# Kernel optimization log

Measured on AMD Instinct MI355X. Metric: run time of the kernel, lower is better.

The kernel has to match this reference:

```python
import jax, jax.numpy as jnp
import numpy as np

B, S = 32, 128
E_NUM, SKILL, D_K, D_E, D_A = 4000, 256, 128, 128, 128
AT_NUM, IT_NUM = 1000, 1000
GAMMA = 0.03


def _lin(key, out_d, in_d):
    # xavier-normal style init
    w = jax.random.normal(key, (out_d, in_d), jnp.float32) * (2.0 / (in_d + out_d)) ** 0.5
    b = jnp.zeros((out_d,), jnp.float32)
    return w, b


def setup_inputs() -> dict:
    key = jax.random.key(0)
    ks = jax.random.split(key, 16)
    exercise_id = jax.random.randint(ks[0], (B, S), 0, E_NUM, jnp.int32)
    ans_time = jax.random.randint(ks[1], (B, S), 0, AT_NUM, jnp.int32)
    interval_time = jax.random.randint(ks[2], (B, S), 0, IT_NUM, jnp.int32)
    answer_value = jax.random.randint(ks[3], (B, S), 0, 2, jnp.int32)
    # enhanced q-matrix: binary with zeros replaced by gamma
    qmask = jax.random.bernoulli(ks[4], 0.1, (E_NUM, SKILL))
    q_matrix = jnp.where(qmask, 1.0, GAMMA).astype(jnp.float32)
    ex_table = jax.random.normal(ks[5], (E_NUM, D_E), jnp.float32)
    at_table = jax.random.normal(ks[6], (AT_NUM, D_K), jnp.float32)
    it_table = jax.random.normal(ks[7], (IT_NUM, D_K), jnp.float32)
    W1, b1 = _lin(ks[8], D_K, D_E + D_K + D_A)   # learning_embed_layer
    Wl, bl = _lin(ks[9], D_K, 4 * D_K)           # learning_layer
    Wg, bg = _lin(ks[10], D_K, 4 * D_K)          # learning_gate
    Wf, bf = _lin(ks[11], D_K, 3 * D_K)          # forgetting_gate
    Wp, bp = _lin(ks[12], D_K, 2 * D_K)          # predicting_layer
    # xavier-uniform initial knowledge state, shared across batch
    lim = (6.0 / (SKILL + D_K)) ** 0.5
    h0 = jax.random.uniform(ks[13], (SKILL, D_K), jnp.float32, -lim, lim)
    return {"exercise_id": exercise_id, "ans_time": ans_time,
            "interval_time": interval_time, "answer_value": answer_value,
            "q_matrix": q_matrix, "ex_table": ex_table, "at_table": at_table,
            "it_table": it_table, "W1": W1, "b1": b1, "Wl": Wl, "bl": bl,
            "Wg": Wg, "bg": bg, "Wf": Wf, "bf": bf, "Wp": Wp, "bp": bp, "h0": h0}


def _forward(exercise_id, ans_time, interval_time, answer_value, q_matrix,
             ex_table, at_table, it_table, W1, b1, Wl, bl, Wg, bg, Wf, bf,
             Wp, bp, h0):
    b, s = exercise_id.shape
    ex = ex_table[exercise_id]                       # (B,S,d_e)
    at = at_table[ans_time]                          # (B,S,d_k)
    it = it_table[interval_time]                     # (B,S,d_k)
    ans = jnp.broadcast_to(answer_value.astype(ex.dtype)[..., None], (b, s, D_A))
    le = jnp.concatenate([ex, at, ans], -1) @ W1.T + b1   # learning embedding (B,S,d_k)
    kv = q_matrix[exercise_id]                       # knowledge vectors (B,S,skill)

    h_pre = jnp.broadcast_to(h0, (b,) + h0.shape)    # (B,skill,d_k)
    h_tilde_pre = jnp.einsum('bs,bsd->bd', kv[:, 0], h_pre)
    learning_pre = jnp.zeros((b, D_K), ex.dtype)

    def step(carry, xs):
        h_pre, h_tilde_pre, learning_pre = carry
        lv, itv, kv_t, kv_next, ex_next = xs
        x4 = jnp.concatenate([learning_pre, itv, lv, h_tilde_pre], -1)
        lg = jnp.tanh(x4 @ Wl.T + bl)
        gate = jax.nn.sigmoid(x4 @ Wg.T + bg)
        LG = gate * (lg + 1.0) * 0.5                 # (B,d_k)
        LG_tilde = kv_t[:, :, None] * LG[:, None, :] # outer product addressing (B,skill,d_k)
        x3 = jnp.concatenate([h_pre,
                              jnp.broadcast_to(LG[:, None, :], h_pre.shape),
                              jnp.broadcast_to(itv[:, None, :], h_pre.shape)], -1)
        f = jax.nn.sigmoid(x3 @ Wf.T + bf)           # forget gate per skill
        h = LG_tilde + f * h_pre                     # updated knowledge state
        h_tilde = jnp.einsum('bs,bsd->bd', kv_next, h)
        pred = jax.nn.sigmoid(jnp.concatenate([ex_next, h_tilde], -1) @ Wp.T + bp)
        return (h, h_tilde, lv), pred

    sw = lambda a: jnp.swapaxes(a, 0, 1)
    xs = (sw(le[:, :-1]), sw(it[:, 1:]), sw(kv[:, :-1]), sw(kv[:, 1:]), sw(ex[:, 1:]))
    _, preds = jax.lax.scan(step, (h_pre, h_tilde_pre, learning_pre), xs)
    return jnp.swapaxes(preds, 0, 1)                 # (B, S-1, d_k)


def reference(exercise_id, ans_time, interval_time, answer_value, q_matrix,
              ex_table, at_table, it_table, W1, b1, Wl, bl, Wg, bg, Wf, bf,
              Wp, bp, h0):
    return _forward(exercise_id, ans_time, interval_time, answer_value, q_matrix,
                    ex_table, at_table, it_table, W1, b1, Wl, bl, Wg, bg, Wf, bf,
                    Wp, bp, h0)
```

## Files before the change

kernel.cpp:

```cpp
#include <hip/hip_runtime.h>

typedef unsigned int u32;
typedef unsigned short u16;
typedef unsigned long long u64;
typedef u16 u16x8 __attribute__((ext_vector_type(8)));
typedef u16 u16x4 __attribute__((ext_vector_type(4)));
typedef __bf16 bf16x8 __attribute__((ext_vector_type(8)));
typedef __bf16 bf16x4v __attribute__((ext_vector_type(4)));
typedef float f32x4 __attribute__((ext_vector_type(4)));
typedef float f32x2 __attribute__((ext_vector_type(2)));

#define B_SZ 32
#define S_SZ 128
#define T_SZ 127
#define DK 128
#define SKILL 256
#define SQTR 64
#define RL 136
#define PP 68
#define NPAIR 8
#define SPIN_CAP (1 << 18)

__device__ __forceinline__ u16x4 cvt4(f32x4 v) {
    return __builtin_bit_cast(u16x4, __builtin_convertvector(v, bf16x4v));
}
__device__ __forceinline__ u16x8 cvt8(f32x4 a, f32x4 b) {
    u16x4 x = cvt4(a), y = cvt4(b);
    u16x8 r;
    r[0]=x[0]; r[1]=x[1]; r[2]=x[2]; r[3]=x[3];
    r[4]=y[0]; r[5]=y[1]; r[6]=y[2]; r[7]=y[3];
    return r;
}
__device__ __forceinline__ u16 bfu(float x) {
    return __builtin_bit_cast(u16, (__bf16)x);
}
__device__ __forceinline__ float sigm(float x) {
    float e = __builtin_amdgcn_exp2f(-1.44269504f * x);
    return __builtin_amdgcn_rcpf(1.f + e);
}
__device__ __forceinline__ float tanh_f(float x) {
    float e = __builtin_amdgcn_exp2f(-2.88539008f * x);
    return 2.f * __builtin_amdgcn_rcpf(1.f + e) - 1.f;
}
__device__ __forceinline__ f32x4 mfma16(u16x8 a, u16x8 bb, f32x4 c) {
    return __builtin_amdgcn_mfma_f32_16x16x32_bf16(
        __builtin_bit_cast(bf16x8, a), __builtin_bit_cast(bf16x8, bb), c, 0, 0, 0);
}
__device__ __forceinline__ float pval(u64 p) {
    return __builtin_bit_cast(float, (u32)p);
}

__global__ __launch_bounds__(256) void k_le(
    const int* __restrict__ eid, const int* __restrict__ atime,
    const int* __restrict__ ansv, const float* __restrict__ ex_t,
    const float* __restrict__ at_t, const float* __restrict__ W1,
    const float* __restrict__ b1, float* __restrict__ le_ws)
{
    const int tid = threadIdx.x;
    const int o = tid & 127;
    const int gi = __builtin_amdgcn_readfirstlane(tid >> 7);
    const int p0 = blockIdx.x * NPAIR + gi * 4;
    int eP[4], aP[4];
    float avP[4];
    #pragma unroll
    for (int i = 0; i < 4; ++i) {
        int p = p0 + i, b = p / T_SZ, t = p - b * T_SZ;
        int idx = b * S_SZ + t;
        eP[i] = eid[idx];
        aP[i] = atime[idx];
        avP[i] = (float)ansv[idx];
    }
    const float* wr = W1 + o * 384;
    const float bias = b1[o];
    float acc[4] = {bias, bias, bias, bias};
    #pragma unroll 4
    for (int k4 = 0; k4 < 32; ++k4) {
        f32x4 w = *(const f32x4*)(wr + 4 * k4);
        #pragma unroll
        for (int i = 0; i < 4; ++i) {
            f32x4 x = *(const f32x4*)(ex_t + eP[i] * DK + 4 * k4);
            acc[i] += w[0] * x[0] + w[1] * x[1] + w[2] * x[2] + w[3] * x[3];
        }
    }
    #pragma unroll 4
    for (int k4 = 32; k4 < 64; ++k4) {
        f32x4 w = *(const f32x4*)(wr + 4 * k4);
        #pragma unroll
        for (int i = 0; i < 4; ++i) {
            f32x4 x = *(const f32x4*)(at_t + aP[i] * DK + 4 * k4 - 128);
            acc[i] += w[0] * x[0] + w[1] * x[1] + w[2] * x[2] + w[3] * x[3];
        }
    }
    float wsum = 0.f;
    #pragma unroll 4
    for (int k4 = 64; k4 < 96; ++k4) {
        f32x4 w = *(const f32x4*)(wr + 4 * k4);
        wsum += w[0] + w[1] + w[2] + w[3];
    }
    #pragma unroll
    for (int i = 0; i < 4; ++i)
        le_ws[(p0 + i) * DK + o] = acc[i] + avP[i] * wsum;
}

__global__ __launch_bounds__(256) void k_pre(
    const int* __restrict__ itime, const float* __restrict__ it_t,
    const float* __restrict__ Wl, const float* __restrict__ blv,
    const float* __restrict__ Wg, const float* __restrict__ bgv,
    const float* __restrict__ Wf, const float* __restrict__ bfv,
    const float* __restrict__ le_ws,
    float* __restrict__ PRE_l, float* __restrict__ PRE_g, float* __restrict__ PRE_f)
{
    const int tid = threadIdx.x;
    const int o = tid & 127;
    const int gi = __builtin_amdgcn_readfirstlane(tid >> 7);
    const int p0 = blockIdx.x * NPAIR + gi * 4;
    int ivP[4], lpOff[4];
    float mP[4];
    #pragma unroll
    for (int i = 0; i < 4; ++i) {
        int p = p0 + i, b = p / T_SZ, t = p - b * T_SZ;
        ivP[i] = itime[b * S_SZ + t + 1];
        mP[i] = (t == 0) ? 0.f : 1.f;
        lpOff[i] = ((t == 0) ? p : p - 1) * DK;
    }
    const float* wl = Wl + o * 512;
    const float* wg = Wg + o * 512;
    const float bl0 = blv[o], bg0 = bgv[o];
    float al[4] = {bl0, bl0, bl0, bl0};
    float ag[4] = {bg0, bg0, bg0, bg0};
    #pragma unroll 4
    for (int k4 = 0; k4 < 32; ++k4) {
        f32x4 w  = *(const f32x4*)(wl + 4 * k4);
        f32x4 w2 = *(const f32x4*)(wg + 4 * k4);
        #pragma unroll
        for (int i = 0; i < 4; ++i) {
            f32x4 x = *(const f32x4*)(le_ws + lpOff[i] + 4 * k4);
            #pragma unroll
            for (int j = 0; j < 4; ++j) {
                float xv = x[j] * mP[i];
                al[i] += w[j] * xv;
                ag[i] += w2[j] * xv;
            }
        }
    }
    #pragma unroll 4
    for (int k4 = 0; k4 < 32; ++k4) {
        f32x4 w  = *(const f32x4*)(wl + 128 + 4 * k4);
        f32x4 w2 = *(const f32x4*)(wg + 128 + 4 * k4);
        #pragma unroll
        for (int i = 0; i < 4; ++i) {
            f32x4 x = *(const f32x4*)(it_t + ivP[i] * DK + 4 * k4);
            #pragma unroll
            for (int j = 0; j < 4; ++j) {
                al[i] += w[j] * x[j];
                ag[i] += w2[j] * x[j];
            }
        }
    }
    #pragma unroll 4
    for (int k4 = 0; k4 < 32; ++k4) {
        f32x4 w  = *(const f32x4*)(wl + 256 + 4 * k4);
        f32x4 w2 = *(const f32x4*)(wg + 256 + 4 * k4);
        #pragma unroll
        for (int i = 0; i < 4; ++i) {
            f32x4 x = *(const f32x4*)(le_ws + (p0 + i) * DK + 4 * k4);
            #pragma unroll
            for (int j = 0; j < 4; ++j) {
                al[i] += w[j] * x[j];
                ag[i] += w2[j] * x[j];
            }
        }
    }
    const float bf0 = bfv[o];
    float af[4] = {bf0, bf0, bf0, bf0};
    const float* wf = Wf + o * 384 + 256;
    #pragma unroll 4
    for (int k4 = 0; k4 < 32; ++k4) {
        f32x4 w = *(const f32x4*)(wf + 4 * k4);
        #pragma unroll
        for (int i = 0; i < 4; ++i) {
            f32x4 x = *(const f32x4*)(it_t + ivP[i] * DK + 4 * k4);
            af[i] += w[0] * x[0] + w[1] * x[1] + w[2] * x[2] + w[3] * x[3];
        }
    }
    #pragma unroll
    for (int i = 0; i < 4; ++i) {
        size_t idx = (size_t)(p0 + i) * DK + o;
        PRE_l[idx] = al[i];
        PRE_g[idx] = ag[i];
        PRE_f[idx] = af[i];
    }
}

__global__ __launch_bounds__(512, 1) void k_main(
    const int* __restrict__ eid, const float* __restrict__ qmat,
    const float* __restrict__ Wl, const float* __restrict__ Wg,
    const float* __restrict__ Wf, const float* __restrict__ h0,
    const float* __restrict__ PRE_l, const float* __restrict__ PRE_g,
    const float* __restrict__ PRE_f, float* __restrict__ ht_ws,
    u64* __restrict__ xbuf)
{
    extern __shared__ char smem[];
    u16*   hS   = (u16*)smem;
    float* part = (float*)(smem + 17408);
    u16*   htbf = (u16*)(smem + 52224);
    u16*   LGb  = (u16*)(smem + 52736);
    float* LGf  = (float*)(smem + 53248);
    float* cS   = (float*)(smem + 53760);

    const int b    = blockIdx.x;
    const int qid  = blockIdx.y;
    const int tid  = threadIdx.x;
    const int w    = tid >> 6;
    const int lane = tid & 63;
    const int quad = lane >> 4;
    const int l4   = lane & 15;
    const int ih   = w & 1;
    const int jh   = w >> 1;

    u64* xq = xbuf + (size_t)b * 1024;
    const int qa = (qid + 1) & 3, qb2 = (qid + 2) & 3, qc = (qid + 3) & 3;

    u16x8 afr[4][4];
    #pragma unroll
    for (int mt = 0; mt < 4; ++mt)
        #pragma unroll
        for (int kt = 0; kt < 4; ++kt) {
            const float* p = Wf + (64 * ih + 16 * mt + l4) * 384 + 32 * kt + quad * 8;
            afr[mt][kt] = cvt8(*(const f32x4*)p, *(const f32x4*)(p + 4));
        }
    u16x8 azf[2][4];
    #pragma unroll
    for (int mt = 0; mt < 2; ++mt)
        #pragma unroll
        for (int kt = 0; kt < 4; ++kt) {
            int d = 16 * w + 8 * mt + (l4 >> 1);
            const float* base = (l4 & 1) ? Wg : Wl;
            const float* p = base + d * 512 + 384 + 32 * kt + quad * 8;
            azf[mt][kt] = cvt8(*(const f32x4*)p, *(const f32x4*)(p + 4));
        }
    u16x8 acf[4];
    #pragma unroll
    for (int kt = 0; kt < 4; ++kt) {
        const float* p = Wf + (16 * w + l4) * 384 + 128 + 32 * kt + quad * 8;
        acf[kt] = cvt8(*(const f32x4*)p, *(const f32x4*)(p + 4));
    }

    const int sl = 16 * jh + l4;
    f32x4 hreg[4];
    #pragma unroll
    for (int mt = 0; mt < 4; ++mt) {
        int d0 = 64 * ih + 16 * mt + quad * 4;
        f32x4 hv = *(const f32x4*)(h0 + (SQTR * qid + sl) * DK + d0);
        hreg[mt] = hv;
        *(u16x4*)(hS + sl * RL + d0) = cvt4(hv);
    }

    float kvt = qmat[eid[b * S_SZ] * SKILL + SQTR * qid + sl];

    f32x4 accF[4];

    {
        float htp[16];
        #pragma unroll
        for (int mt = 0; mt < 4; ++mt)
            #pragma unroll
            for (int r = 0; r < 4; ++r)
                htp[mt * 4 + r] = kvt * hreg[mt][r];
        #pragma unroll
        for (int mt = 0; mt < 4; ++mt)
            #pragma unroll
            for (int r = 0; r < 4; ++r)
                part[(64 * ih + 16 * mt + quad * 4 + r) * PP + jh * 16 + l4] = htp[mt * 4 + r];
        __syncthreads();
        int d = tid >> 2, kq = tid & 3;
        const float* pp = part + d * PP + kq * 16;
        float v = 0.f;
        #pragma unroll
        for (int i4 = 0; i4 < 4; ++i4) {
            f32x4 x = *(const f32x4*)(pp + 4 * i4);
            v += x[0] + x[1] + x[2] + x[3];
        }
        v += __shfl_xor(v, 1, 64);
        v += __shfl_xor(v, 2, 64);
        if (kq == 0) {
            u64 pkt = ((u64)1u << 32) | (u64)__builtin_bit_cast(u32, v);
            __hip_atomic_store(xq + qid * 256 + 128 + d, pkt,
                               __ATOMIC_RELAXED, __HIP_MEMORY_SCOPE_AGENT);
        }
        asm volatile("" ::: "memory");
        #pragma unroll
        for (int mt = 0; mt < 4; ++mt)
            accF[mt] = (f32x4){0.f, 0.f, 0.f, 0.f};
        {
            const u16* bp = hS + sl * RL + quad * 8;
            u16x8 bfr[4];
            #pragma unroll
            for (int kt = 0; kt < 4; ++kt) bfr[kt] = *(const u16x8*)(bp + kt * 32);
            #pragma unroll
            for (int mt = 0; mt < 4; ++mt)
                #pragma unroll
                for (int kt = 0; kt < 4; ++kt)
                    accF[mt] = mfma16(afr[mt][kt], bfr[kt], accF[mt]);
        }
        if (kq == 0) {
            u64 pa, pb, pc;
            int spins = 0;
            do {
                pa = __hip_atomic_load(xq + qa * 256 + 128 + d, __ATOMIC_RELAXED, __HIP_MEMORY_SCOPE_AGENT);
                pb = __hip_atomic_load(xq + qb2 * 256 + 128 + d, __ATOMIC_RELAXED, __HIP_MEMORY_SCOPE_AGENT);
                pc = __hip_atomic_load(xq + qc * 256 + 128 + d, __ATOMIC_RELAXED, __HIP_MEMORY_SCOPE_AGENT);
                if ((u32)(pa >> 32) >= 1u && (u32)(pb >> 32) >= 1u && (u32)(pc >> 32) >= 1u) break;
                if (spins > 64) __builtin_amdgcn_s_sleep(1);
            } while (++spins < SPIN_CAP);
            float va = pval(pa), vb = pval(pb), vc = pval(pc);
            float v0 = (qid == 0) ? v : (qid == 3) ? va : (qid == 2) ? vb : vc;
            float v1 = (qid == 1) ? v : (qid == 0) ? va : (qid == 3) ? vb : vc;
            float v2 = (qid == 2) ? v : (qid == 1) ? va : (qid == 0) ? vb : vc;
            float v3 = (qid == 3) ? v : (qid == 2) ? va : (qid == 1) ? vb : vc;
            float vt = ((v0 + v1) + v2) + v3;
            float hf = (float)(__bf16)vt;
            htbf[d] = bfu(vt);
            htbf[128 + d] = bfu(vt - hf);
        }
        __syncthreads();
    }

    for (int t = 0; t < T_SZ; ++t) {
        const size_t tb = (size_t)(b * T_SZ + t) * DK;
        float kvn = qmat[eid[b * S_SZ + t + 1] * SKILL + SQTR * qid + sl];
        f32x2 pl[2], pg[2];
        #pragma unroll
        for (int mt = 0; mt < 2; ++mt) {
            int d0 = 16 * w + 8 * mt + 2 * quad;
            pl[mt] = *(const f32x2*)(PRE_l + tb + d0);
            pg[mt] = *(const f32x2*)(PRE_g + tb + d0);
        }
        f32x4 pf = *(const f32x4*)(PRE_f + tb + 16 * w + quad * 4);

        f32x4 accZ[2];
        accZ[0] = (f32x4){0.f, 0.f, 0.f, 0.f};
        accZ[1] = (f32x4){0.f, 0.f, 0.f, 0.f};
        #pragma unroll
        for (int kt = 0; kt < 4; ++kt) {
            u16x8 bh = *(const u16x8*)(htbf + 32 * kt + quad * 8);
            u16x8 bl = *(const u16x8*)(htbf + 128 + 32 * kt + quad * 8);
            #pragma unroll
            for (int mt = 0; mt < 2; ++mt) {
                accZ[mt] = mfma16(azf[mt][kt], bh, accZ[mt]);
                accZ[mt] = mfma16(azf[mt][kt], bl, accZ[mt]);
            }
        }
        #pragma unroll
        for (int mt = 0; mt < 2; ++mt) {
            u32 hpack = 0, lpack = 0;
            f32x2 fpack;
            #pragma unroll
            for (int rp = 0; rp < 2; ++rp) {
                float zl = accZ[mt][2 * rp] + pl[mt][rp];
                float zg = accZ[mt][2 * rp + 1] + pg[mt][rp];
                float LGv = sigm(zg) * (tanh_f(zl) + 1.f) * 0.5f;
                float hif = (float)(__bf16)LGv;
                hpack |= ((u32)bfu(LGv)) << (16 * rp);
                lpack |= ((u32)bfu(LGv - hif)) << (16 * rp);
                fpack[rp] = LGv;
            }
            if (l4 == 0) {
                int d0 = 16 * w + 8 * mt + 2 * quad;
                *(u32*)(LGb + d0) = hpack;
                *(u32*)(LGb + 128 + d0) = lpack;
                *(f32x2*)(LGf + d0) = fpack;
            }
        }
        __syncthreads();

        {
            f32x4 accC = (f32x4){0.f, 0.f, 0.f, 0.f};
            #pragma unroll
            for (int kt = 0; kt < 4; ++kt) {
                u16x8 bh = *(const u16x8*)(LGb + 32 * kt + quad * 8);
                u16x8 bl = *(const u16x8*)(LGb + 128 + 32 * kt + quad * 8);
                accC = mfma16(acf[kt], bh, accC);
                accC = mfma16(acf[kt], bl, accC);
            }
            accC += pf;
            if (l4 == 0) *(f32x4*)(cS + 16 * w + quad * 4) = accC;
        }
        __syncthreads();

        float htp[16];
        #pragma unroll
        for (int mt = 0; mt < 4; ++mt) {
            int d0 = 64 * ih + 16 * mt + quad * 4;
            f32x4 lg = *(const f32x4*)(LGf + d0);
            f32x4 cc = *(const f32x4*)(cS + d0);
            f32x4 hv;
            #pragma unroll
            for (int r = 0; r < 4; ++r) {
                float f = sigm(accF[mt][r] + cc[r]);
                float hn = kvt * lg[r] + f * hreg[mt][r];
                hreg[mt][r] = hn;
                htp[mt * 4 + r] = kvn * hn;
                hv[r] = hn;
            }
            *(u16x4*)(hS + sl * RL + d0) = cvt4(hv);
        }
        #pragma unroll
        for (int mt = 0; mt < 4; ++mt)
            #pragma unroll
            for (int r = 0; r < 4; ++r)
                part[(64 * ih + 16 * mt + quad * 4 + r) * PP + jh * 16 + l4] = htp[mt * 4 + r];
        kvt = kvn;
        __syncthreads();

        {
            int d = tid >> 2, kq = tid & 3;
            const float* pp = part + d * PP + kq * 16;
            float v = 0.f;
            #pragma unroll
            for (int i4 = 0; i4 < 4; ++i4) {
                f32x4 x = *(const f32x4*)(pp + 4 * i4);
                v += x[0] + x[1] + x[2] + x[3];
            }
            v += __shfl_xor(v, 1, 64);
            v += __shfl_xor(v, 2, 64);
            const int slot = t & 1;
            const u32 seq = (u32)(t + 2);
            if (kq == 0) {
                u64 pkt = ((u64)seq << 32) | (u64)__builtin_bit_cast(u32, v);
                __hip_atomic_store(xq + qid * 256 + slot * 128 + d, pkt,
                                   __ATOMIC_RELAXED, __HIP_MEMORY_SCOPE_AGENT);
            }
            asm volatile("" ::: "memory");
            #pragma unroll
            for (int mt = 0; mt < 4; ++mt)
                accF[mt] = (f32x4){0.f, 0.f, 0.f, 0.f};
            {
                const u16* bp = hS + sl * RL + quad * 8;
                u16x8 bfr[4];
                #pragma unroll
                for (int kt = 0; kt < 4; ++kt) bfr[kt] = *(const u16x8*)(bp + kt * 32);
                #pragma unroll
                for (int mt = 0; mt < 4; ++mt)
                    #pragma unroll
                    for (int kt = 0; kt < 4; ++kt)
                        accF[mt] = mfma16(afr[mt][kt], bfr[kt], accF[mt]);
            }
            if (kq == 0) {
                u64 pa, pb, pc;
                int spins = 0;
                do {
                    pa = __hip_atomic_load(xq + qa * 256 + slot * 128 + d, __ATOMIC_RELAXED, __HIP_MEMORY_SCOPE_AGENT);
                    pb = __hip_atomic_load(xq + qb2 * 256 + slot * 128 + d, __ATOMIC_RELAXED, __HIP_MEMORY_SCOPE_AGENT);
                    pc = __hip_atomic_load(xq + qc * 256 + slot * 128 + d, __ATOMIC_RELAXED, __HIP_MEMORY_SCOPE_AGENT);
                    if ((u32)(pa >> 32) >= seq && (u32)(pb >> 32) >= seq && (u32)(pc >> 32) >= seq) break;
                    if (spins > 64) __builtin_amdgcn_s_sleep(1);
                } while (++spins < SPIN_CAP);
                float va = pval(pa), vb = pval(pb), vc = pval(pc);
                float v0 = (qid == 0) ? v : (qid == 3) ? va : (qid == 2) ? vb : vc;
                float v1 = (qid == 1) ? v : (qid == 0) ? va : (qid == 3) ? vb : vc;
                float v2 = (qid == 2) ? v : (qid == 1) ? va : (qid == 0) ? vb : vc;
                float v3 = (qid == 3) ? v : (qid == 2) ? va : (qid == 1) ? vb : vc;
                float vt = ((v0 + v1) + v2) + v3;
                float hf = (float)(__bf16)vt;
                htbf[d] = bfu(vt);
                htbf[128 + d] = bfu(vt - hf);
                if (qid == 0) ht_ws[tb + d] = vt;
            }
        }
        __syncthreads();
    }
}

__global__ __launch_bounds__(256) void k_pred(
    const int* __restrict__ eid, const float* __restrict__ ex_t,
    const float* __restrict__ Wp, const float* __restrict__ bpv,
    const float* __restrict__ ht_ws, float* __restrict__ out)
{
    const int tid = threadIdx.x;
    const int o = tid & 127;
    const int gi = __builtin_amdgcn_readfirstlane(tid >> 7);
    const int p0 = blockIdx.x * NPAIR + gi * 4;
    int eP[4];
    #pragma unroll
    for (int i = 0; i < 4; ++i) {
        int p = p0 + i, b = p / T_SZ, t = p - b * T_SZ;
        eP[i] = eid[b * S_SZ + t + 1];
    }
    const float* wr = Wp + o * 256;
    const float bias = bpv[o];
    float acc[4] = {bias, bias, bias, bias};
    #pragma unroll 4
    for (int k4 = 0; k4 < 32; ++k4) {
        f32x4 w = *(const f32x4*)(wr + 4 * k4);
        #pragma unroll
        for (int i = 0; i < 4; ++i) {
            f32x4 x = *(const f32x4*)(ex_t + eP[i] * DK + 4 * k4);
            acc[i] += w[0] * x[0] + w[1] * x[1] + w[2] * x[2] + w[3] * x[3];
        }
    }
    #pragma unroll 4
    for (int k4 = 32; k4 < 64; ++k4) {
        f32x4 w = *(const f32x4*)(wr + 4 * k4);
        #pragma unroll
        for (int i = 0; i < 4; ++i) {
            f32x4 x = *(const f32x4*)(ht_ws + (size_t)(p0 + i) * DK + 4 * k4 - 128);
            acc[i] += w[0] * x[0] + w[1] * x[1] + w[2] * x[2] + w[3] * x[3];
        }
    }
    #pragma unroll
    for (int i = 0; i < 4; ++i)
        out[(size_t)(p0 + i) * DK + o] = sigm(acc[i]);
}

extern "C" void kernel_launch(void* const* d_in, const int* in_sizes, int n_in,
                              void* d_out, int out_size, void* d_ws, size_t ws_size,
                              hipStream_t stream) {
    const int* eid     = (const int*)d_in[0];
    const int* atime   = (const int*)d_in[1];
    const int* itime   = (const int*)d_in[2];
    const int* ansv    = (const int*)d_in[3];
    const float* qmat  = (const float*)d_in[4];
    const float* ex_t  = (const float*)d_in[5];
    const float* at_t  = (const float*)d_in[6];
    const float* it_t  = (const float*)d_in[7];
    const float* W1    = (const float*)d_in[8];
    const float* b1    = (const float*)d_in[9];
    const float* Wl    = (const float*)d_in[10];
    const float* blv   = (const float*)d_in[11];
    const float* Wg    = (const float*)d_in[12];
    const float* bgv   = (const float*)d_in[13];
    const float* Wf    = (const float*)d_in[14];
    const float* bfv   = (const float*)d_in[15];
    const float* Wp    = (const float*)d_in[16];
    const float* bpv   = (const float*)d_in[17];
    const float* h0    = (const float*)d_in[18];
    float* out = (float*)d_out;

    const size_t SZ = (size_t)B_SZ * T_SZ * DK;
    float* wsf   = (float*)d_ws;
    float* le_ws = wsf;
    float* PRE_l = wsf + SZ;
    float* PRE_g = wsf + 2 * SZ;
    float* PRE_f = wsf + 3 * SZ;
    float* ht_ws = wsf + 4 * SZ;
    u64* xbuf = (u64*)le_ws;

    hipFuncSetAttribute((const void*)k_main,
                        hipFuncAttributeMaxDynamicSharedMemorySize, 86016);

    dim3 gaux(508);
    k_le  <<<gaux, 256, 0, stream>>>(eid, atime, ansv, ex_t, at_t, W1, b1, le_ws);
    k_pre <<<gaux, 256, 0, stream>>>(itime, it_t, Wl, blv, Wg, bgv, Wf, bfv,
                                     le_ws, PRE_l, PRE_g, PRE_f);
    hipMemsetAsync(xbuf, 0, (size_t)B_SZ * 1024 * sizeof(u64), stream);
    k_main<<<dim3(B_SZ, 4), 512, 86016, stream>>>(eid, qmat, Wl, Wg, Wf, h0,
                                                  PRE_l, PRE_g, PRE_f, ht_ws,
                                                  xbuf);
    k_pred<<<gaux, 256, 0, stream>>>(eid, ex_t, Wp, bpv, ht_ws, out);
}
```

Before: 593.6 us.

## Fuse prediction layer into recurrent main kernel and widen aux kernels per thread

The separate k_pred launch is removed. Each main-kernel block now computes its 32-output slice of the prediction for the previous step at the start of every timestep, using Wp rows held in registers, h_tilde kept in shared memory, and shuffle reductions. Separately, k_le and k_pre drop to 128-thread blocks, with each thread handling 8 pairs instead of 4. This saves a launch and the ht_ws round trip, but adds work to the serial critical path of the recurrent loop and may lower parallelism in the aux kernels.

```diff
diff --git a/kernel.cpp b/kernel.cpp
--- a/kernel.cpp
+++ b/kernel.cpp
@@ -49,21 +49,22 @@
 __device__ __forceinline__ float pval(u64 p) {
     return __builtin_bit_cast(float, (u32)p);
 }
-
-__global__ __launch_bounds__(256) void k_le(
+__device__ __forceinline__ float dot4(f32x4 w, f32x4 x) {
+    return w[0] * x[0] + w[1] * x[1] + w[2] * x[2] + w[3] * x[3];
+}
+
+__global__ __launch_bounds__(128) void k_le(
     const int* __restrict__ eid, const int* __restrict__ atime,
     const int* __restrict__ ansv, const float* __restrict__ ex_t,
     const float* __restrict__ at_t, const float* __restrict__ W1,
     const float* __restrict__ b1, float* __restrict__ le_ws)
 {
-    const int tid = threadIdx.x;
-    const int o = tid & 127;
-    const int gi = __builtin_amdgcn_readfirstlane(tid >> 7);
-    const int p0 = blockIdx.x * NPAIR + gi * 4;
-    int eP[4], aP[4];
-    float avP[4];
-    #pragma unroll
-    for (int i = 0; i < 4; ++i) {
+    const int o = threadIdx.x;
+    const int p0 = blockIdx.x * NPAIR;
+    int eP[NPAIR], aP[NPAIR];
+    float avP[NPAIR];
+    #pragma unroll
+    for (int i = 0; i < NPAIR; ++i) {
         int p = p0 + i, b = p / T_SZ, t = p - b * T_SZ;
         int idx = b * S_SZ + t;
         eP[i] = eid[idx];
@@ -72,23 +73,25 @@
     }
     const float* wr = W1 + o * 384;
     const float bias = b1[o];
-    float acc[4] = {bias, bias, bias, bias};
-    #pragma unroll 4
+    float acc[NPAIR];
+    #pragma unroll
+    for (int i = 0; i < NPAIR; ++i) acc[i] = bias;
+    #pragma unroll 2
     for (int k4 = 0; k4 < 32; ++k4) {
         f32x4 w = *(const f32x4*)(wr + 4 * k4);
         #pragma unroll
-        for (int i = 0; i < 4; ++i) {
+        for (int i = 0; i < NPAIR; ++i) {
             f32x4 x = *(const f32x4*)(ex_t + eP[i] * DK + 4 * k4);
-            acc[i] += w[0] * x[0] + w[1] * x[1] + w[2] * x[2] + w[3] * x[3];
-        }
-    }
-    #pragma unroll 4
+            acc[i] += dot4(w, x);
+        }
+    }
+    #pragma unroll 2
     for (int k4 = 32; k4 < 64; ++k4) {
         f32x4 w = *(const f32x4*)(wr + 4 * k4);
         #pragma unroll
-        for (int i = 0; i < 4; ++i) {
+        for (int i = 0; i < NPAIR; ++i) {
             f32x4 x = *(const f32x4*)(at_t + aP[i] * DK + 4 * k4 - 128);
-            acc[i] += w[0] * x[0] + w[1] * x[1] + w[2] * x[2] + w[3] * x[3];
+            acc[i] += dot4(w, x);
         }
     }
     float wsum = 0.f;
@@ -98,11 +101,11 @@
         wsum += w[0] + w[1] + w[2] + w[3];
     }
     #pragma unroll
-    for (int i = 0; i < 4; ++i)
+    for (int i = 0; i < NPAIR; ++i)
         le_ws[(p0 + i) * DK + o] = acc[i] + avP[i] * wsum;
 }
 
-__global__ __launch_bounds__(256) void k_pre(
+__global__ __launch_bounds__(128) void k_pre(
     const int* __restrict__ itime, const float* __restrict__ it_t,
     const float* __restrict__ Wl, const float* __restrict__ blv,
     const float* __restrict__ Wg, const float* __restrict__ bgv,
@@ -110,14 +113,12 @@
     const float* __restrict__ le_ws,
     float* __restrict__ PRE_l, float* __restrict__ PRE_g, float* __restrict__ PRE_f)
 {
-    const int tid = threadIdx.x;
-    const int o = tid & 127;
-    const int gi = __builtin_amdgcn_readfirstlane(tid >> 7);
-    const int p0 = blockIdx.x * NPAIR + gi * 4;
-    int ivP[4], lpOff[4];
-    float mP[4];
-    #pragma unroll
-    for (int i = 0; i < 4; ++i) {
+    const int o = threadIdx.x;
+    const int p0 = blockIdx.x * NPAIR;
+    int ivP[NPAIR], lpOff[NPAIR];
+    float mP[NPAIR];
+    #pragma unroll
+    for (int i = 0; i < NPAIR; ++i) {
         int p = p0 + i, b = p / T_SZ, t = p - b * T_SZ;
         ivP[i] = itime[b * S_SZ + t + 1];
         mP[i] = (t == 0) ? 0.f : 1.f;
@@ -126,14 +127,15 @@
     const float* wl = Wl + o * 512;
     const float* wg = Wg + o * 512;
     const float bl0 = blv[o], bg0 = bgv[o];
-    float al[4] = {bl0, bl0, bl0, bl0};
-    float ag[4] = {bg0, bg0, bg0, bg0};
-    #pragma unroll 4
+    float al[NPAIR], ag[NPAIR];
+    #pragma unroll
+    for (int i = 0; i < NPAIR; ++i) { al[i] = bl0; ag[i] = bg0; }
+    #pragma unroll 2
     for (int k4 = 0; k4 < 32; ++k4) {
         f32x4 w  = *(const f32x4*)(wl + 4 * k4);
         f32x4 w2 = *(const f32x4*)(wg + 4 * k4);
         #pragma unroll
-        for (int i = 0; i < 4; ++i) {
+        for (int i = 0; i < NPAIR; ++i) {
             f32x4 x = *(const f32x4*)(le_ws + lpOff[i] + 4 * k4);
             #pragma unroll
             for (int j = 0; j < 4; ++j) {
@@ -143,12 +145,12 @@
             }
         }
     }
-    #pragma unroll 4
+    #pragma unroll 2
     for (int k4 = 0; k4 < 32; ++k4) {
         f32x4 w  = *(const f32x4*)(wl + 128 + 4 * k4);
         f32x4 w2 = *(const f32x4*)(wg + 128 + 4 * k4);
         #pragma unroll
-        for (int i = 0; i < 4; ++i) {
+        for (int i = 0; i < NPAIR; ++i) {
             f32x4 x = *(const f32x4*)(it_t + ivP[i] * DK + 4 * k4);
             #pragma unroll
             for (int j = 0; j < 4; ++j) {
@@ -157,12 +159,12 @@
             }
         }
     }
-    #pragma unroll 4
+    #pragma unroll 2
     for (int k4 = 0; k4 < 32; ++k4) {
         f32x4 w  = *(const f32x4*)(wl + 256 + 4 * k4);
         f32x4 w2 = *(const f32x4*)(wg + 256 + 4 * k4);
         #pragma unroll
-        for (int i = 0; i < 4; ++i) {
+        for (int i = 0; i < NPAIR; ++i) {
             f32x4 x = *(const f32x4*)(le_ws + (p0 + i) * DK + 4 * k4);
             #pragma unroll
             for (int j = 0; j < 4; ++j) {
@@ -172,19 +174,21 @@
         }
     }
     const float bf0 = bfv[o];
-    float af[4] = {bf0, bf0, bf0, bf0};
+    float af[NPAIR];
+    #pragma unroll
+    for (int i = 0; i < NPAIR; ++i) af[i] = bf0;
     const float* wf = Wf + o * 384 + 256;
-    #pragma unroll 4
+    #pragma unroll 2
     for (int k4 = 0; k4 < 32; ++k4) {
         f32x4 w = *(const f32x4*)(wf + 4 * k4);
         #pragma unroll
-        for (int i = 0; i < 4; ++i) {
+        for (int i = 0; i < NPAIR; ++i) {
             f32x4 x = *(const f32x4*)(it_t + ivP[i] * DK + 4 * k4);
-            af[i] += w[0] * x[0] + w[1] * x[1] + w[2] * x[2] + w[3] * x[3];
-        }
-    }
-    #pragma unroll
-    for (int i = 0; i < 4; ++i) {
+            af[i] += dot4(w, x);
+        }
+    }
+    #pragma unroll
+    for (int i = 0; i < NPAIR; ++i) {
         size_t idx = (size_t)(p0 + i) * DK + o;
         PRE_l[idx] = al[i];
         PRE_g[idx] = ag[i];
@@ -197,8 +201,9 @@
     const float* __restrict__ Wl, const float* __restrict__ Wg,
     const float* __restrict__ Wf, const float* __restrict__ h0,
     const float* __restrict__ PRE_l, const float* __restrict__ PRE_g,
-    const float* __restrict__ PRE_f, float* __restrict__ ht_ws,
-    u64* __restrict__ xbuf)
+    const float* __restrict__ PRE_f, const float* __restrict__ ex_t,
+    const float* __restrict__ Wp, const float* __restrict__ bpv,
+    float* __restrict__ out, u64* __restrict__ xbuf)
 {
     extern __shared__ char smem[];
     u16*   hS   = (u16*)smem;
@@ -207,6 +212,7 @@
     u16*   LGb  = (u16*)(smem + 52736);
     float* LGf  = (float*)(smem + 53248);
     float* cS   = (float*)(smem + 53760);
+    float* htf  = (float*)(smem + 54272);
 
     const int b    = blockIdx.x;
     const int qid  = blockIdx.y;
@@ -221,6 +227,16 @@
     u64* xq = xbuf + (size_t)b * 1024;
     const int qa = (qid + 1) & 3, qb2 = (qid + 2) & 3, qc = (qid + 3) & 3;
 
+    const int pj = tid >> 4;
+    const int pc = tid & 15;
+    f32x4 wp4[4];
+    {
+        const float* wpr = Wp + (32 * qid + pj) * 256 + pc * 16;
+        #pragma unroll
+        for (int i = 0; i < 4; ++i) wp4[i] = *(const f32x4*)(wpr + 4 * i);
+    }
+    const float bp = bpv[32 * qid + pj];
+
     u16x8 afr[4][4];
     #pragma unroll
     for (int mt = 0; mt < 4; ++mt)
@@ -293,10 +309,10 @@
         for (int mt = 0; mt < 4; ++mt)
             accF[mt] = (f32x4){0.f, 0.f, 0.f, 0.f};
         {
-            const u16* bp = hS + sl * RL + quad * 8;
+            const u16* bp2 = hS + sl * RL + quad * 8;
             u16x8 bfr[4];
             #pragma unroll
-            for (int kt = 0; kt < 4; ++kt) bfr[kt] = *(const u16x8*)(bp + kt * 32);
+            for (int kt = 0; kt < 4; ++kt) bfr[kt] = *(const u16x8*)(bp2 + kt * 32);
             #pragma unroll
             for (int mt = 0; mt < 4; ++mt)
                 #pragma unroll
@@ -304,16 +320,16 @@
                     accF[mt] = mfma16(afr[mt][kt], bfr[kt], accF[mt]);
         }
         if (kq == 0) {
-            u64 pa, pb, pc;
+            u64 pa, pb, pc2;
             int spins = 0;
             do {
-                pa = __hip_atomic_load(xq + qa * 256 + 128 + d, __ATOMIC_RELAXED, __HIP_MEMORY_SCOPE_AGENT);
-                pb = __hip_atomic_load(xq + qb2 * 256 + 128 + d, __ATOMIC_RELAXED, __HIP_MEMORY_SCOPE_AGENT);
-                pc = __hip_atomic_load(xq + qc * 256 + 128 + d, __ATOMIC_RELAXED, __HIP_MEMORY_SCOPE_AGENT);
-                if ((u32)(pa >> 32) >= 1u && (u32)(pb >> 32) >= 1u && (u32)(pc >> 32) >= 1u) break;
+                pa  = __hip_atomic_load(xq + qa * 256 + 128 + d, __ATOMIC_RELAXED, __HIP_MEMORY_SCOPE_AGENT);
+                pb  = __hip_atomic_load(xq + qb2 * 256 + 128 + d, __ATOMIC_RELAXED, __HIP_MEMORY_SCOPE_AGENT);
+                pc2 = __hip_atomic_load(xq + qc * 256 + 128 + d, __ATOMIC_RELAXED, __HIP_MEMORY_SCOPE_AGENT);
+                if ((u32)(pa >> 32) >= 1u && (u32)(pb >> 32) >= 1u && (u32)(pc2 >> 32) >= 1u) break;
                 if (spins > 64) __builtin_amdgcn_s_sleep(1);
             } while (++spins < SPIN_CAP);
-            float va = pval(pa), vb = pval(pb), vc = pval(pc);
+            float va = pval(pa), vb = pval(pb), vc = pval(pc2);
             float v0 = (qid == 0) ? v : (qid == 3) ? va : (qid == 2) ? vb : vc;
             float v1 = (qid == 1) ? v : (qid == 0) ? va : (qid == 3) ? vb : vc;
             float v2 = (qid == 2) ? v : (qid == 1) ? va : (qid == 0) ? vb : vc;
@@ -328,6 +344,31 @@
 
     for (int t = 0; t < T_SZ; ++t) {
         const size_t tb = (size_t)(b * T_SZ + t) * DK;
+
+        if (t > 0) {
+            int epid = eid[b * S_SZ + t];
+            float pacc;
+            if (pc < 8) {
+                const float* xr = ex_t + epid * DK + pc * 16;
+                pacc  = dot4(wp4[0], *(const f32x4*)xr);
+                pacc += dot4(wp4[1], *(const f32x4*)(xr + 4));
+                pacc += dot4(wp4[2], *(const f32x4*)(xr + 8));
+                pacc += dot4(wp4[3], *(const f32x4*)(xr + 12));
+            } else {
+                const float* xr = htf + (pc - 8) * 16;
+                pacc  = dot4(wp4[0], *(const f32x4*)xr);
+                pacc += dot4(wp4[1], *(const f32x4*)(xr + 4));
+                pacc += dot4(wp4[2], *(const f32x4*)(xr + 8));
+                pacc += dot4(wp4[3], *(const f32x4*)(xr + 12));
+            }
+            pacc += __shfl_xor(pacc, 1, 64);
+            pacc += __shfl_xor(pacc, 2, 64);
+            pacc += __shfl_xor(pacc, 4, 64);
+            pacc += __shfl_xor(pacc, 8, 64);
+            if (pc == 0)
+                out[(size_t)(b * T_SZ + t - 1) * DK + 32 * qid + pj] = sigm(pacc + bp);
+        }
+
         float kvn = qmat[eid[b * S_SZ + t + 1] * SKILL + SQTR * qid + sl];
         f32x2 pl[2], pg[2];
         #pragma unroll
@@ -436,10 +477,10 @@
             for (int mt = 0; mt < 4; ++mt)
                 accF[mt] = (f32x4){0.f, 0.f, 0.f, 0.f};
             {
-                const u16* bp = hS + sl * RL + quad * 8;
+                const u16* bp2 = hS + sl * RL + quad * 8;
                 u16x8 bfr[4];
                 #pragma unroll
-                for (int kt = 0; kt < 4; ++kt) bfr[kt] = *(const u16x8*)(bp + kt * 32);
+                for (int kt = 0; kt < 4; ++kt) bfr[kt] = *(const u16x8*)(bp2 + kt * 32);
                 #pragma unroll
                 for (int mt = 0; mt < 4; ++mt)
                     #pragma unroll
@@ -447,16 +488,16 @@
                         accF[mt] = mfma16(afr[mt][kt], bfr[kt], accF[mt]);
             }
             if (kq == 0) {
-                u64 pa, pb, pc;
+                u64 pa, pb, pc2;
                 int spins = 0;
                 do {
-                    pa = __hip_atomic_load(xq + qa * 256 + slot * 128 + d, __ATOMIC_RELAXED, __HIP_MEMORY_SCOPE_AGENT);
-                    pb = __hip_atomic_load(xq + qb2 * 256 + slot * 128 + d, __ATOMIC_RELAXED, __HIP_MEMORY_SCOPE_AGENT);
-                    pc = __hip_atomic_load(xq + qc * 256 + slot * 128 + d, __ATOMIC_RELAXED, __HIP_MEMORY_SCOPE_AGENT);
-                    if ((u32)(pa >> 32) >= seq && (u32)(pb >> 32) >= seq && (u32)(pc >> 32) >= seq) break;
+                    pa  = __hip_atomic_load(xq + qa * 256 + slot * 128 + d, __ATOMIC_RELAXED, __HIP_MEMORY_SCOPE_AGENT);
+                    pb  = __hip_atomic_load(xq + qb2 * 256 + slot * 128 + d, __ATOMIC_RELAXED, __HIP_MEMORY_SCOPE_AGENT);
+                    pc2 = __hip_atomic_load(xq + qc * 256 + slot * 128 + d, __ATOMIC_RELAXED, __HIP_MEMORY_SCOPE_AGENT);
+                    if ((u32)(pa >> 32) >= seq && (u32)(pb >> 32) >= seq && (u32)(pc2 >> 32) >= seq) break;
                     if (spins > 64) __builtin_amdgcn_s_sleep(1);
                 } while (++spins < SPIN_CAP);
-                float va = pval(pa), vb = pval(pb), vc = pval(pc);
+                float va = pval(pa), vb = pval(pb), vc = pval(pc2);
                 float v0 = (qid == 0) ? v : (qid == 3) ? va : (qid == 2) ? vb : vc;
                 float v1 = (qid == 1) ? v : (qid == 0) ? va : (qid == 3) ? vb : vc;
                 float v2 = (qid == 2) ? v : (qid == 1) ? va : (qid == 0) ? vb : vc;
@@ -465,52 +506,35 @@
                 float hf = (float)(__bf16)vt;
                 htbf[d] = bfu(vt);
                 htbf[128 + d] = bfu(vt - hf);
-                if (qid == 0) ht_ws[tb + d] = vt;
+                htf[d] = vt;
             }
         }
         __syncthreads();
     }
-}
-
-__global__ __launch_bounds__(256) void k_pred(
-    const int* __restrict__ eid, const float* __restrict__ ex_t,
-    const float* __restrict__ Wp, const float* __restrict__ bpv,
-    const float* __restrict__ ht_ws, float* __restrict__ out)
-{
-    const int tid = threadIdx.x;
-    const int o = tid & 127;
-    const int gi = __builtin_amdgcn_readfirstlane(tid >> 7);
-    const int p0 = blockIdx.x * NPAIR + gi * 4;
-    int eP[4];
-    #pragma unroll
-    for (int i = 0; i < 4; ++i) {
-        int p = p0 + i, b = p / T_SZ, t = p - b * T_SZ;
-        eP[i] = eid[b * S_SZ + t + 1];
-    }
-    const float* wr = Wp + o * 256;
-    const float bias = bpv[o];
-    float acc[4] = {bias, bias, bias, bias};
-    #pragma unroll 4
-    for (int k4 = 0; k4 < 32; ++k4) {
-        f32x4 w = *(const f32x4*)(wr + 4 * k4);
-        #pragma unroll
-        for (int i = 0; i < 4; ++i) {
-            f32x4 x = *(const f32x4*)(ex_t + eP[i] * DK + 4 * k4);
-            acc[i] += w[0] * x[0] + w[1] * x[1] + w[2] * x[2] + w[3] * x[3];
-        }
-    }
-    #pragma unroll 4
-    for (int k4 = 32; k4 < 64; ++k4) {
-        f32x4 w = *(const f32x4*)(wr + 4 * k4);
-        #pragma unroll
-        for (int i = 0; i < 4; ++i) {
-            f32x4 x = *(const f32x4*)(ht_ws + (size_t)(p0 + i) * DK + 4 * k4 - 128);
-            acc[i] += w[0] * x[0] + w[1] * x[1] + w[2] * x[2] + w[3] * x[3];
-        }
-    }
-    #pragma unroll
-    for (int i = 0; i < 4; ++i)
-        out[(size_t)(p0 + i) * DK + o] = sigm(acc[i]);
+
+    {
+        int epid = eid[b * S_SZ + T_SZ];
+        float pacc;
+        if (pc < 8) {
+            const float* xr = ex_t + epid * DK + pc * 16;
+            pacc  = dot4(wp4[0], *(const f32x4*)xr);
+            pacc += dot4(wp4[1], *(const f32x4*)(xr + 4));
+            pacc += dot4(wp4[2], *(const f32x4*)(xr + 8));
+            pacc += dot4(wp4[3], *(const f32x4*)(xr + 12));
+        } else {
+            const float* xr = htf + (pc - 8) * 16;
+            pacc  = dot4(wp4[0], *(const f32x4*)xr);
+            pacc += dot4(wp4[1], *(const f32x4*)(xr + 4));
+            pacc += dot4(wp4[2], *(const f32x4*)(xr + 8));
+            pacc += dot4(wp4[3], *(const f32x4*)(xr + 12));
+        }
+        pacc += __shfl_xor(pacc, 1, 64);
+        pacc += __shfl_xor(pacc, 2, 64);
+        pacc += __shfl_xor(pacc, 4, 64);
+        pacc += __shfl_xor(pacc, 8, 64);
+        if (pc == 0)
+            out[(size_t)(b * T_SZ + T_SZ - 1) * DK + 32 * qid + pj] = sigm(pacc + bp);
+    }
 }
 
 extern "C" void kernel_launch(void* const* d_in, const int* in_sizes, int n_in,
@@ -543,19 +567,17 @@
     float* PRE_l = wsf + SZ;
     float* PRE_g = wsf + 2 * SZ;
     float* PRE_f = wsf + 3 * SZ;
-    float* ht_ws = wsf + 4 * SZ;
     u64* xbuf = (u64*)le_ws;
 
     hipFuncSetAttribute((const void*)k_main,
                         hipFuncAttributeMaxDynamicSharedMemorySize, 86016);
 
     dim3 gaux(508);
-    k_le  <<<gaux, 256, 0, stream>>>(eid, atime, ansv, ex_t, at_t, W1, b1, le_ws);
-    k_pre <<<gaux, 256, 0, stream>>>(itime, it_t, Wl, blv, Wg, bgv, Wf, bfv,
+    k_le  <<<gaux, 128, 0, stream>>>(eid, atime, ansv, ex_t, at_t, W1, b1, le_ws);
+    k_pre <<<gaux, 128, 0, stream>>>(itime, it_t, Wl, blv, Wg, bgv, Wf, bfv,
                                      le_ws, PRE_l, PRE_g, PRE_f);
     hipMemsetAsync(xbuf, 0, (size_t)B_SZ * 1024 * sizeof(u64), stream);
     k_main<<<dim3(B_SZ, 4), 512, 86016, stream>>>(eid, qmat, Wl, Wg, Wf, h0,
-                                                  PRE_l, PRE_g, PRE_f, ht_ws,
-                                                  xbuf);
-    k_pred<<<gaux, 256, 0, stream>>>(eid, ex_t, Wp, bpv, ht_ws, out);
-}
+                                                  PRE_l, PRE_g, PRE_f,
+                                                  ex_t, Wp, bpv, out, xbuf);
+}
```

After: 662.9 us. 11.7% more time.
